# Kernel tuning notes

Measured on AMD Instinct MI355X. Metric: run time of the kernel, lower is better.

## Reference

```python
import jax, jax.numpy as jnp
import numpy as np

NUM_TIME_BLOCKS = 32  # P
B, L, D = 32, 4096, 256


def setup_inputs() -> dict:
    key = jax.random.key(0)
    k1, k2 = jax.random.split(key)
    x = jax.random.normal(k1, (B, L, D), dtype=jnp.float32)
    # normalized timestamps in [0, 1), matching linspace(0, 1.001, P+1) bin edges
    time_steps = jax.random.uniform(k2, (B, L), dtype=jnp.float32)
    return {"x": x, "time_steps": time_steps}


def reference(x, time_steps):
    # Bin edges identical to torch.linspace(0.0, 1.001, P+1)
    blocks = jnp.linspace(0.0, 1.001, NUM_TIME_BLOCKS + 1, dtype=jnp.float32)
    ls = blocks[:-1]  # (P,) left edges (inclusive)
    rs = blocks[1:]   # (P,) right edges (exclusive)
    ts = time_steps[..., None]                      # (B, L, 1)
    # one-hot bucket membership mask, (B, L, P); a token falls in exactly one bin
    mask = ((ts >= ls) & (ts < rs)).astype(x.dtype)
    # sum x over sequence positions within each time bucket -> (B, P, D)
    new_x = jnp.einsum('blp,bld->bpd', mask, x)
    return new_x, time_steps
```

## Files before the change

kernel.cpp:

```cpp
#include <hip/hip_runtime.h>


#define Bk 32
#define Lk 4096
#define Dk 256
#define Pk 32

__device__ __forceinline__ int bucket_of(float tv) {
    const double step = 1.001 / 32.0;
    int p = (int)(tv * (float)(32.0 / 1.001));
    p = p < 0 ? 0 : (p > 31 ? 31 : p);
    while (p > 0 && tv < (float)((double)p * step)) --p;
    while (p < 31 && tv >= (float)((double)(p + 1) * step)) ++p;
    return p;
}

__global__ __launch_bounds__(512) void tc_bucketize(
        const float* __restrict__ ts,
        int* __restrict__ list,
        int* __restrict__ bounds,
        float* __restrict__ ts_out) {
    __shared__ int cnt[Pk];
    __shared__ int off[Pk];
    const int b = blockIdx.x;
    const int t = threadIdx.x;

    if (t < Pk) cnt[t] = 0;
    __syncthreads();

    int pv[8];
#pragma unroll
    for (int k = 0; k < 8; ++k) {
        const int l = t + k * 512;
        const float tv = ts[(size_t)b * Lk + l];
        ts_out[(size_t)b * Lk + l] = tv;
        const int p = bucket_of(tv);
        pv[k] = p;
        atomicAdd(&cnt[p], 1);
    }
    __syncthreads();

    if (t == 0) {
        int s = 0;
        for (int p = 0; p < Pk; ++p) {
            off[p] = s;
            bounds[b * (Pk + 1) + p] = s;
            s += cnt[p];
        }
        bounds[b * (Pk + 1) + Pk] = s;
    }
    __syncthreads();

#pragma unroll
    for (int k = 0; k < 8; ++k) {
        const int l = t + k * 512;
        const int idx = atomicAdd(&off[pv[k]], 1);
        list[(size_t)b * Lk + idx] = l;
    }
}

__global__ __launch_bounds__(256) void tc_gather(
        const float* __restrict__ x,
        const int* __restrict__ list,
        const int* __restrict__ bounds,
        float* __restrict__ out) {
    __shared__ int rows[Lk];
    __shared__ float red[4 * Dk];

    const int p = blockIdx.x;
    const int b = blockIdx.y;
    const int t = threadIdx.x;
    const int w = t >> 6;
    const int lane = t & 63;
    const int col4 = lane << 2;

    const int start = bounds[b * (Pk + 1) + p];
    const int cnt = bounds[b * (Pk + 1) + p + 1] - start;

    for (int i = t; i < cnt; i += 256)
        rows[i] = list[(size_t)b * Lk + start + i];
    __syncthreads();

    const float* xb = x + (size_t)b * Lk * Dk;
    float4 acc = make_float4(0.f, 0.f, 0.f, 0.f);
    for (int i = w; i < cnt; i += 4) {
        const int row = rows[i];
        const float4 v = *(const float4*)(xb + (size_t)row * Dk + col4);
        acc.x += v.x; acc.y += v.y; acc.z += v.z; acc.w += v.w;
    }

    *(float4*)&red[t * 4] = acc;
    __syncthreads();
    if (w == 0) {
        float4 r = *(float4*)&red[lane * 4];
#pragma unroll
        for (int ww = 1; ww < 4; ++ww) {
            const float4 o = *(const float4*)&red[(ww * 64 + lane) * 4];
            r.x += o.x; r.y += o.y; r.z += o.z; r.w += o.w;
        }
        *(float4*)(out + ((size_t)b * Pk + p) * Dk + col4) = r;
    }
}

extern "C" void kernel_launch(void* const* d_in, const int* in_sizes, int n_in,
                              void* d_out, int out_size, void* d_ws, size_t ws_size,
                              hipStream_t stream) {
    const float* x  = (const float*)d_in[0];
    const float* ts = (const float*)d_in[1];
    float* out = (float*)d_out;
    float* ts_out = out + (size_t)Bk * Pk * Dk;

    int* list   = (int*)d_ws;
    int* bounds = list + (size_t)Bk * Lk;

    tc_bucketize<<<Bk, 512, 0, stream>>>(ts, list, bounds, ts_out);
    dim3 grid(Pk, Bk);
    tc_gather<<<grid, 256, 0, stream>>>(x, list, bounds, out);
}
```

Before: 204.4 us.

## Fuse bucketize and gather into one kernel with per-block timestamp scan

Removes the separate bucketize kernel and its global list/bounds workspace. Each (bucket, batch) block now scans all timestamps of its batch itself and appends the matching row indices to shared memory with an atomic counter. The gather loop is also unrolled by two with separate accumulators to keep more loads in flight. In exchange, every block redundantly reads and bucketizes 4096 timestamps (32x duplicated work), and the row order, and hence summation order, becomes nondeterministic.

```diff
diff --git a/kernel.cpp b/kernel.cpp
--- a/kernel.cpp
+++ b/kernel.cpp
@@ -15,56 +15,13 @@
     return p;
 }
 
-__global__ __launch_bounds__(512) void tc_bucketize(
+__global__ __launch_bounds__(256) void tc_fused(
+        const float* __restrict__ x,
         const float* __restrict__ ts,
-        int* __restrict__ list,
-        int* __restrict__ bounds,
+        float* __restrict__ out,
         float* __restrict__ ts_out) {
-    __shared__ int cnt[Pk];
-    __shared__ int off[Pk];
-    const int b = blockIdx.x;
-    const int t = threadIdx.x;
-
-    if (t < Pk) cnt[t] = 0;
-    __syncthreads();
-
-    int pv[8];
-#pragma unroll
-    for (int k = 0; k < 8; ++k) {
-        const int l = t + k * 512;
-        const float tv = ts[(size_t)b * Lk + l];
-        ts_out[(size_t)b * Lk + l] = tv;
-        const int p = bucket_of(tv);
-        pv[k] = p;
-        atomicAdd(&cnt[p], 1);
-    }
-    __syncthreads();
-
-    if (t == 0) {
-        int s = 0;
-        for (int p = 0; p < Pk; ++p) {
-            off[p] = s;
-            bounds[b * (Pk + 1) + p] = s;
-            s += cnt[p];
-        }
-        bounds[b * (Pk + 1) + Pk] = s;
-    }
-    __syncthreads();
-
-#pragma unroll
-    for (int k = 0; k < 8; ++k) {
-        const int l = t + k * 512;
-        const int idx = atomicAdd(&off[pv[k]], 1);
-        list[(size_t)b * Lk + idx] = l;
-    }
-}
-
-__global__ __launch_bounds__(256) void tc_gather(
-        const float* __restrict__ x,
-        const int* __restrict__ list,
-        const int* __restrict__ bounds,
-        float* __restrict__ out) {
     __shared__ int rows[Lk];
+    __shared__ int nrows;
     __shared__ float red[4 * Dk];
 
     const int p = blockIdx.x;
@@ -74,22 +31,42 @@
     const int lane = t & 63;
     const int col4 = lane << 2;
 
-    const int start = bounds[b * (Pk + 1) + p];
-    const int cnt = bounds[b * (Pk + 1) + p + 1] - start;
-
-    for (int i = t; i < cnt; i += 256)
-        rows[i] = list[(size_t)b * Lk + start + i];
+    if (t == 0) nrows = 0;
     __syncthreads();
 
+    const float* tsb = ts + (size_t)b * Lk;
+#pragma unroll
+    for (int k = 0; k < Lk / 256; ++k) {
+        const int l = t + k * 256;
+        const float tv = tsb[l];
+        if (p == 0) ts_out[(size_t)b * Lk + l] = tv;
+        if (bucket_of(tv) == p) {
+            const int idx = atomicAdd(&nrows, 1);
+            rows[idx] = l;
+        }
+    }
+    __syncthreads();
+    const int cnt = nrows;
+
     const float* xb = x + (size_t)b * Lk * Dk;
-    float4 acc = make_float4(0.f, 0.f, 0.f, 0.f);
-    for (int i = w; i < cnt; i += 4) {
-        const int row = rows[i];
-        const float4 v = *(const float4*)(xb + (size_t)row * Dk + col4);
-        acc.x += v.x; acc.y += v.y; acc.z += v.z; acc.w += v.w;
+    float4 a0 = make_float4(0.f, 0.f, 0.f, 0.f);
+    float4 a1 = make_float4(0.f, 0.f, 0.f, 0.f);
+    int i = w;
+    for (; i + 4 < cnt; i += 8) {
+        const int r0 = rows[i];
+        const int r1 = rows[i + 4];
+        const float4 v0 = *(const float4*)(xb + (size_t)r0 * Dk + col4);
+        const float4 v1 = *(const float4*)(xb + (size_t)r1 * Dk + col4);
+        a0.x += v0.x; a0.y += v0.y; a0.z += v0.z; a0.w += v0.w;
+        a1.x += v1.x; a1.y += v1.y; a1.z += v1.z; a1.w += v1.w;
     }
+    if (i < cnt) {
+        const float4 v = *(const float4*)(xb + (size_t)rows[i] * Dk + col4);
+        a0.x += v.x; a0.y += v.y; a0.z += v.z; a0.w += v.w;
+    }
+    a0.x += a1.x; a0.y += a1.y; a0.z += a1.z; a0.w += a1.w;
 
-    *(float4*)&red[t * 4] = acc;
+    *(float4*)&red[t * 4] = a0;
     __syncthreads();
     if (w == 0) {
         float4 r = *(float4*)&red[lane * 4];
@@ -110,10 +87,6 @@
     float* out = (float*)d_out;
     float* ts_out = out + (size_t)Bk * Pk * Dk;
 
-    int* list   = (int*)d_ws;
-    int* bounds = list + (size_t)Bk * Lk;
-
-    tc_bucketize<<<Bk, 512, 0, stream>>>(ts, list, bounds, ts_out);
     dim3 grid(Pk, Bk);
-    tc_gather<<<grid, 256, 0, stream>>>(x, list, bounds, out);
+    tc_fused<<<grid, 256, 0, stream>>>(x, ts, out, ts_out);
 }
```

Result: no change. 203.6 us (-0.4%).

## Split gather across z-slices with atomic accumulation and unrolled row loads

Applied to the files above, without the earlier changes.

The gather kernel now splits each bucket's row list into 16 contiguous segments, one per wave across 4 z-slices, which quadruples the grid. Each wave issues 8 independent float4 loads per iteration into two accumulators, and the shared-memory staging and reduction are dropped. Partial sums go to the output through float atomics, so the output must first be zeroed with a memset. The change is meant to raise memory-level parallelism and occupancy for this bandwidth-bound gather, at the cost of an extra memset and atomic contention on the output.

```diff
diff --git a/kernel.cpp b/kernel.cpp
--- a/kernel.cpp
+++ b/kernel.cpp
@@ -59,47 +59,59 @@
     }
 }
 
-__global__ __launch_bounds__(256) void tc_gather(
+__global__ __launch_bounds__(256, 6) void tc_gather(
         const float* __restrict__ x,
         const int* __restrict__ list,
         const int* __restrict__ bounds,
         float* __restrict__ out) {
-    __shared__ int rows[Lk];
-    __shared__ float red[4 * Dk];
-
     const int p = blockIdx.x;
     const int b = blockIdx.y;
+    const int s = blockIdx.z;
     const int t = threadIdx.x;
     const int w = t >> 6;
     const int lane = t & 63;
     const int col4 = lane << 2;
+    const int sidx = s * 4 + w;
 
     const int start = bounds[b * (Pk + 1) + p];
     const int cnt = bounds[b * (Pk + 1) + p + 1] - start;
-
-    for (int i = t; i < cnt; i += 256)
-        rows[i] = list[(size_t)b * Lk + start + i];
-    __syncthreads();
+    const int seg = (cnt + 15) >> 4;
+    int i = start + sidx * seg;
+    const int iend = min(i + seg, start + cnt);
 
     const float* xb = x + (size_t)b * Lk * Dk;
-    float4 acc = make_float4(0.f, 0.f, 0.f, 0.f);
-    for (int i = w; i < cnt; i += 4) {
-        const int row = rows[i];
-        const float4 v = *(const float4*)(xb + (size_t)row * Dk + col4);
-        acc.x += v.x; acc.y += v.y; acc.z += v.z; acc.w += v.w;
+    const int* lb = list + (size_t)b * Lk;
+
+    float4 a0 = make_float4(0.f, 0.f, 0.f, 0.f);
+    float4 a1 = make_float4(0.f, 0.f, 0.f, 0.f);
+
+    for (; i + 8 <= iend; i += 8) {
+        int r[8];
+#pragma unroll
+        for (int j = 0; j < 8; ++j) r[j] = lb[i + j];
+        float4 v[8];
+#pragma unroll
+        for (int j = 0; j < 8; ++j)
+            v[j] = *(const float4*)(xb + (size_t)r[j] * Dk + col4);
+#pragma unroll
+        for (int j = 0; j < 8; j += 2) {
+            a0.x += v[j].x;     a0.y += v[j].y;
+            a0.z += v[j].z;     a0.w += v[j].w;
+            a1.x += v[j + 1].x; a1.y += v[j + 1].y;
+            a1.z += v[j + 1].z; a1.w += v[j + 1].w;
+        }
     }
+    for (; i < iend; ++i) {
+        const float4 v = *(const float4*)(xb + (size_t)lb[i] * Dk + col4);
+        a0.x += v.x; a0.y += v.y; a0.z += v.z; a0.w += v.w;
+    }
+    a0.x += a1.x; a0.y += a1.y; a0.z += a1.z; a0.w += a1.w;
 
-    *(float4*)&red[t * 4] = acc;
-    __syncthreads();
-    if (w == 0) {
-        float4 r = *(float4*)&red[lane * 4];
-#pragma unroll
-        for (int ww = 1; ww < 4; ++ww) {
-            const float4 o = *(const float4*)&red[(ww * 64 + lane) * 4];
-            r.x += o.x; r.y += o.y; r.z += o.z; r.w += o.w;
-        }
-        *(float4*)(out + ((size_t)b * Pk + p) * Dk + col4) = r;
-    }
+    float* op = out + ((size_t)b * Pk + p) * Dk + col4;
+    unsafeAtomicAdd(&op[0], a0.x);
+    unsafeAtomicAdd(&op[1], a0.y);
+    unsafeAtomicAdd(&op[2], a0.z);
+    unsafeAtomicAdd(&op[3], a0.w);
 }
 
 extern "C" void kernel_launch(void* const* d_in, const int* in_sizes, int n_in,
@@ -113,7 +125,9 @@
     int* list   = (int*)d_ws;
     int* bounds = list + (size_t)Bk * Lk;
 
+    hipMemsetAsync(out, 0, (size_t)Bk * Pk * Dk * sizeof(float), stream);
+
     tc_bucketize<<<Bk, 512, 0, stream>>>(ts, list, bounds, ts_out);
-    dim3 grid(Pk, Bk);
+    dim3 grid(Pk, Bk, 4);
     tc_gather<<<grid, 256, 0, stream>>>(x, list, bounds, out);
 }
```

Result: slower. 225.4 us (+10.3%).
